# Performance work log

Hardware: AMD Instinct MI355X
Metric: run time of the kernel (lower is better)

The kernel has to match this reference:

```python
import jax, jax.numpy as jnp
import numpy as np
from jax import lax

B, A, K = 16, 200000, 300          # batch, anchors, NMS candidate cap
THR_CONF, THR_NMS = 0.5, 0.3
VAR0, VAR1 = 0.1, 0.2              # RetinaFace decode variances


def setup_inputs() -> dict:
    key = jax.random.key(0)
    k1, k2, k3, k4, k5 = jax.random.split(key, 5)
    p_loc = jax.random.normal(k1, (B, A, 4), jnp.float32) * 0.5
    p_conf = jax.random.normal(k2, (B, A, 1), jnp.float32) - 2.0
    p_landms = jax.random.normal(k3, (B, A, 10), jnp.float32) * 0.5
    cxy = jax.random.uniform(k4, (A, 2), jnp.float32)
    wh = 0.01 + 0.09 * jax.random.uniform(k5, (A, 2), jnp.float32)
    anchors = jnp.concatenate([cxy, wh], axis=-1)   # [A,4] cx,cy,w,h in [0,1]
    return {"p_loc": p_loc, "p_conf": p_conf, "p_landms": p_landms, "anchors": anchors}


def _decode_boxes_ltrb(anchors, loc):
    # fix_bbox: cxy = a_cxy + loc[:2]*0.1*a_wh ; wh = a_wh * exp(loc[2:]*0.2)
    a = anchors[None]                              # [1,A,4]
    cxy = a[..., :2] + loc[..., :2] * VAR0 * a[..., 2:]
    wh = a[..., 2:] * jnp.exp(loc[..., 2:] * VAR1)
    half = 0.5 * wh
    return jnp.concatenate([cxy - half, cxy + half], axis=-1)  # xywh2ltrb -> [B,A,4]


def _decode_keypoints(anchors, landms):
    # fix_keypoints: 5 points, each a_cxy + d*0.1*a_wh (computed in original fwd; unused in outputs)
    a = anchors[None]
    d = landms.reshape(landms.shape[0], landms.shape[1], 5, 2)
    kp = a[..., None, :2] + d * VAR0 * a[..., None, 2:]
    return kp.reshape(landms.shape)


def _iou_matrix(b):  # b [K,4] ltrb -> [K,K]
    lt = jnp.maximum(b[:, None, :2], b[None, :, :2])
    rb = jnp.minimum(b[:, None, 2:], b[None, :, 2:])
    wh = jnp.clip(rb - lt, 0.0)
    inter = wh[..., 0] * wh[..., 1]
    area = jnp.clip(b[:, 2] - b[:, 0], 0.0) * jnp.clip(b[:, 3] - b[:, 1], 0.0)
    union = area[:, None] + area[None, :] - inter
    return inter / jnp.maximum(union, 1e-9)


def _nms_keep(boxes, valid):
    # boxes already sorted by descending score; greedy NMS over K candidates
    iou = _iou_matrix(boxes)
    idx = jnp.arange(K)
    def body(i, keep):
        sup = keep[i] & (iou[i] > THR_NMS) & (idx > i)
        return keep & ~sup
    return lax.fori_loop(0, K, body, valid)


def reference(p_loc, p_conf, p_landms, anchors):
    scores = jax.nn.sigmoid(p_conf[..., 0])                     # [B,A]
    boxes_ltrb = _decode_boxes_ltrb(anchors, p_loc)             # [B,A,4]
    _ = _decode_keypoints(anchors, p_landms)                    # faithful dead compute

    mask = scores >= THR_CONF
    masked_scores = jnp.where(mask, scores, 0.0)
    top_scores, top_idx = lax.top_k(masked_scores, K)           # [B,K] sorted desc
    top_boxes = jnp.take_along_axis(boxes_ltrb, top_idx[..., None], axis=1)  # [B,K,4]
    valid = top_scores >= THR_CONF

    keep = jax.vmap(_nms_keep)(top_boxes, valid)                # [B,K] bool
    keep_f = keep.astype(top_scores.dtype)

    ids_batch2 = jnp.where(keep, jnp.broadcast_to(jnp.arange(B)[:, None], (B, K)), -1).reshape(-1)
    p_boxes_ltrb2 = (top_boxes * keep_f[..., None]).reshape(-1, 4)
    p_scores2 = (top_scores * keep_f).reshape(-1)
    p_labels2 = keep_f.reshape(-1)   # original labels are all ones; zero on padded slots
    return ids_batch2, p_boxes_ltrb2, p_labels2, p_scores2, keep.reshape(-1)
```

## Files before the change

kernel.cpp:

```cpp
#include <hip/hip_runtime.h>
#include <cstdint>

typedef unsigned int u32;
typedef unsigned long long u64;

#define B 16
#define A 200000
#define K 300
#define NREG 196

__global__ __launch_bounds__(256) void scan_kernel(const float* __restrict__ p_conf,
                                                   u64* __restrict__ cand,
                                                   u32* __restrict__ cnt) {
    __shared__ u64 lbuf[1024];
    __shared__ u32 lcnt;
    const int b  = blockIdx.y;
    const int bx = blockIdx.x;
    const int f4 = bx * 256 + threadIdx.x;

    if (threadIdx.x == 0) lcnt = 0;
    __syncthreads();

    if (f4 < A / 4) {
        const float4 c4 = ((const float4*)(p_conf + (size_t)b * A))[f4];
        const float xs[4] = {c4.x, c4.y, c4.z, c4.w};
        #pragma unroll
        for (int e = 0; e < 4; ++e) {
            const float x = xs[e];
            if (x >= -0.001f) {
                float s = 1.0f / (1.0f + expf(-x));
                if (s >= 0.5f) {
                    u32 sb  = __float_as_uint(s);
                    u32 idx = (u32)(f4 * 4 + e);
                    u64 key = ((u64)sb << 32) | (u64)(0xFFFFFFFFu - idx);
                    u32 p = atomicAdd(&lcnt, 1u);
                    lbuf[p] = key;
                }
            }
        }
    }
    __syncthreads();
    const u32 total = lcnt;
    u64* dst = cand + ((size_t)(b * NREG + bx) << 10);
    for (u32 t = threadIdx.x; t < total; t += 256) dst[t] = lbuf[t];
    if (threadIdx.x == 0) cnt[b * NREG + bx] = total;
}

__global__ __launch_bounds__(512) void select_nms_kernel(
    const float* __restrict__ p_loc,
    const float* __restrict__ anchors,
    const u64* __restrict__ cand,
    const u32* __restrict__ cnt,
    float* __restrict__ out) {

    __shared__ u32 scnt[NREG];
    __shared__ u32 hist[512];
    __shared__ u32 sfx[512];
    __shared__ u32 wsum[8];
    __shared__ u64 buf[1024];
    __shared__ u64 skey[K];
    __shared__ float sl[K], st_[K], sr[K], sb_[K], sar[K];
    __shared__ u64 mask[K][5];
    __shared__ u64 validw[5], kcur[5], sup[5];
    __shared__ int s_changed;
    __shared__ u32 sh_cut, sh_m;

    const int b    = blockIdx.x;
    const int tid  = threadIdx.x;
    const int lane = tid & 63;
    const int wv   = tid >> 6;

    hist[tid] = 0;
    {   u64* mf = &mask[0][0];
        for (int i = tid; i < K * 5; i += 512) mf[i] = 0ull; }
    for (int i = tid; i < NREG; i += 512) scnt[i] = cnt[b * NREG + i];
    if (tid == 0) { sh_m = 0; sh_cut = 0; }
    __syncthreads();

    for (int r = wv; r < NREG; r += 8) {
        const u32 kr = scnt[r];
        const u64* p = cand + ((size_t)(b * NREG + r) << 10);
        for (u32 i = lane; i < kr; i += 64) {
            u32 sb  = (u32)(p[i] >> 32);
            u32 bin = min((sb - 0x3F000000u) >> 14, 511u);
            atomicAdd(&hist[bin], 1u);
        }
    }
    __syncthreads();

    u32 s = hist[tid];
    #pragma unroll
    for (int off = 1; off < 64; off <<= 1) {
        u32 t = __shfl_down(s, off, 64);
        if (lane + off < 64) s += t;
    }
    if (lane == 0) wsum[wv] = s;
    __syncthreads();
    u32 tail = 0;
    #pragma unroll
    for (int w = 0; w < 8; ++w) if (w > wv) tail += wsum[w];
    sfx[tid] = s + tail;
    __syncthreads();

    const u32 need = min((u32)K, sfx[0]);
    if (need > 0) {
        if (sfx[tid] >= need && (tid == 511 || sfx[tid + 1] < need)) sh_cut = (u32)tid;
    }
    __syncthreads();

    const u32 cut = sh_cut;
    if (need > 0) {
        for (int r = wv; r < NREG; r += 8) {
            const u32 kr = scnt[r];
            const u64* p = cand + ((size_t)(b * NREG + r) << 10);
            for (u32 i = lane; i < kr; i += 64) {
                u64 kk  = p[i];
                u32 bin = min(((u32)(kk >> 32) - 0x3F000000u) >> 14, 511u);
                if (bin >= cut) {
                    u32 q = atomicAdd(&sh_m, 1u);
                    if (q < 1024) buf[q] = kk;
                }
            }
        }
    }
    __syncthreads();
    const u32 M = min(sh_m, 1024u);

    for (u32 t = tid; t < M; t += 512) {
        const u64 mykey = buf[t];
        u32 r = 0;
        #pragma unroll 4
        for (u32 j = 0; j < M; ++j) r += (buf[j] > mykey) ? 1u : 0u;
        if (r < (u32)K) skey[r] = mykey;
    }
    __syncthreads();

    const u32 S = need;
    float dl = 0.f, dt = 0.f, dr = 0.f, db = 0.f, dsc = 0.f;
    if (tid < K) {
        float ar = 0.f;
        if ((u32)tid < S) {
            u64 kk = skey[tid];
            dsc = __uint_as_float((u32)(kk >> 32));
            u32 aidx = 0xFFFFFFFFu - (u32)(kk & 0xFFFFFFFFull);
            const float4 loc = ((const float4*)p_loc)[(size_t)b * A + aidx];
            const float4 an  = ((const float4*)anchors)[aidx];
            float cx = an.x + loc.x * 0.1f * an.z;
            float cy = an.y + loc.y * 0.1f * an.w;
            float w  = an.z * expf(loc.z * 0.2f);
            float h  = an.w * expf(loc.w * 0.2f);
            dl = cx - 0.5f * w; dt = cy - 0.5f * h;
            dr = cx + 0.5f * w; db = cy + 0.5f * h;
            ar = fmaxf(dr - dl, 0.0f) * fmaxf(db - dt, 0.0f);
        }
        sl[tid] = dl; st_[tid] = dt; sr[tid] = dr; sb_[tid] = db; sar[tid] = ar;
    }
    __syncthreads();

    {
        int r, j0, jstep; bool active;
        if (tid < K) { r = tid;     j0 = r + 1; jstep = (r < 212) ? 2 : 1; active = ((u32)r < S); }
        else         { r = tid - K; j0 = r + 2; jstep = 2;                 active = ((u32)r < S); }
        if (active) {
            const float li = sl[r], ti = st_[r], ri = sr[r], bi = sb_[r], ai = sar[r];
            u64 acc = 0; int wcur = j0 >> 6;
            for (int j = j0; j < (int)S; j += jstep) {
                const int w = j >> 6;
                if (w != wcur) {
                    if (acc) atomicOr(&mask[r][wcur], acc);
                    acc = 0; wcur = w;
                }
                float lt0 = fmaxf(li, sl[j]);
                float lt1 = fmaxf(ti, st_[j]);
                float rb0 = fminf(ri, sr[j]);
                float rb1 = fminf(bi, sb_[j]);
                float iw = fmaxf(rb0 - lt0, 0.0f);
                float ih = fmaxf(rb1 - lt1, 0.0f);
                float inter = iw * ih;
                float uni = ai + sar[j] - inter;
                float iou = inter / fmaxf(uni, 1e-9f);
                if (iou > 0.3f) acc |= (1ull << (j & 63));
            }
            if (acc) atomicOr(&mask[r][wcur], acc);
        }
    }

    u64 m0 = 0, m1 = 0, m2 = 0, m3 = 0, m4 = 0;
    __syncthreads();
    if ((u32)tid < S) {
        m0 = mask[tid][0]; m1 = mask[tid][1]; m2 = mask[tid][2];
        m3 = mask[tid][3]; m4 = mask[tid][4];
    }
    if (tid < 5) {
        int rem = (int)S - tid * 64;
        u64 v = rem <= 0 ? 0ull : (rem >= 64 ? ~0ull : ((1ull << rem) - 1ull));
        validw[tid] = v; kcur[tid] = v;
    }
    __syncthreads();

    for (u32 it = 0; it <= S; ++it) {
        if (tid < 5) sup[tid] = 0;
        if (tid == 0) s_changed = 0;
        __syncthreads();
        u64 c0 = 0, c1 = 0, c2 = 0, c3 = 0, c4 = 0;
        if ((u32)tid < S) {
            u64 kw = kcur[tid >> 6];
            if ((kw >> (tid & 63)) & 1ull) { c0 = m0; c1 = m1; c2 = m2; c3 = m3; c4 = m4; }
        }
        #pragma unroll
        for (int off = 1; off < 64; off <<= 1) {
            c0 |= __shfl_xor(c0, off, 64);
            c1 |= __shfl_xor(c1, off, 64);
            c2 |= __shfl_xor(c2, off, 64);
            c3 |= __shfl_xor(c3, off, 64);
            c4 |= __shfl_xor(c4, off, 64);
        }
        if (lane == 0) {
            if (c0) atomicOr(&sup[0], c0);
            if (c1) atomicOr(&sup[1], c1);
            if (c2) atomicOr(&sup[2], c2);
            if (c3) atomicOr(&sup[3], c3);
            if (c4) atomicOr(&sup[4], c4);
        }
        __syncthreads();
        if (tid < 5) {
            u64 nk = validw[tid] & ~sup[tid];
            if (nk != kcur[tid]) { s_changed = 1; kcur[tid] = nk; }
        }
        __syncthreads();
        if (!s_changed) break;
    }

    if (tid < K) {
        const int g = b * K + tid;
        const bool kept = (kcur[tid >> 6] >> (tid & 63)) & 1ull;
        out[g] = kept ? (float)b : -1.0f;
        float* obox = out + B * K + (size_t)g * 4;
        obox[0] = kept ? dl : 0.0f;
        obox[1] = kept ? dt : 0.0f;
        obox[2] = kept ? dr : 0.0f;
        obox[3] = kept ? db : 0.0f;
        out[B * K * 5 + g] = kept ? 1.0f : 0.0f;
        out[B * K * 6 + g] = kept ? dsc : 0.0f;
        out[B * K * 7 + g] = kept ? 1.0f : 0.0f;
    }
}

extern "C" void kernel_launch(void* const* d_in, const int* in_sizes, int n_in,
                              void* d_out, int out_size, void* d_ws, size_t ws_size,
                              hipStream_t stream) {
    const float* p_loc   = (const float*)d_in[0];
    const float* p_conf  = (const float*)d_in[1];
    const float* anchors = (const float*)d_in[3];
    float* out = (float*)d_out;

    u64* cand = (u64*)d_ws;
    u32* cnt  = (u32*)((char*)d_ws + (size_t)B * NREG * 1024 * 8);

    dim3 gridA(NREG, B);
    scan_kernel<<<gridA, 256, 0, stream>>>(p_conf, cand, cnt);
    select_nms_kernel<<<B, 512, 0, stream>>>(p_loc, anchors, cand, cnt, out);
}
```

Measured before the change: 247.7 us.

## Compact candidates globally and build score histogram in scan kernel

The scan kernel now appends candidates into a per-batch compact buffer through a global atomic counter and accumulates the score histogram in global memory. The select kernel reads the precomputed histogram and a single contiguous candidate list instead of walking 196 sparse per-block regions twice. This takes serial histogram and gather work off the 16-block select kernel. In exchange it adds global atomics, a memset launch, and a fixed cap of 8192 candidates per batch that would silently drop candidates if exceeded.

```diff
diff --git a/kernel.cpp b/kernel.cpp
--- a/kernel.cpp
+++ b/kernel.cpp
@@ -7,16 +7,18 @@
 #define B 16
 #define A 200000
 #define K 300
-#define NREG 196
+#define CAP 8192
+#define NBIN 512
 
 __global__ __launch_bounds__(256) void scan_kernel(const float* __restrict__ p_conf,
                                                    u64* __restrict__ cand,
-                                                   u32* __restrict__ cnt) {
+                                                   u32* __restrict__ cnt,
+                                                   u32* __restrict__ hist) {
     __shared__ u64 lbuf[1024];
     __shared__ u32 lcnt;
+    __shared__ u32 lbase;
     const int b  = blockIdx.y;
-    const int bx = blockIdx.x;
-    const int f4 = bx * 256 + threadIdx.x;
+    const int f4 = blockIdx.x * 256 + threadIdx.x;
 
     if (threadIdx.x == 0) lcnt = 0;
     __syncthreads();
@@ -40,10 +42,16 @@
         }
     }
     __syncthreads();
+    if (threadIdx.x == 0 && lcnt > 0) lbase = atomicAdd(&cnt[b], lcnt);
+    __syncthreads();
     const u32 total = lcnt;
-    u64* dst = cand + ((size_t)(b * NREG + bx) << 10);
-    for (u32 t = threadIdx.x; t < total; t += 256) dst[t] = lbuf[t];
-    if (threadIdx.x == 0) cnt[b * NREG + bx] = total;
+    for (u32 t = threadIdx.x; t < total; t += 256) {
+        const u64 kk = lbuf[t];
+        const u32 bin = min(((u32)(kk >> 32) - 0x3F000000u) >> 14, (u32)(NBIN - 1));
+        atomicAdd(&hist[b * NBIN + bin], 1u);
+        const u32 g = lbase + t;
+        if (g < CAP) cand[(size_t)b * CAP + g] = kk;
+    }
 }
 
 __global__ __launch_bounds__(512) void select_nms_kernel(
@@ -51,11 +59,10 @@
     const float* __restrict__ anchors,
     const u64* __restrict__ cand,
     const u32* __restrict__ cnt,
+    const u32* __restrict__ hist,
     float* __restrict__ out) {
 
-    __shared__ u32 scnt[NREG];
-    __shared__ u32 hist[512];
-    __shared__ u32 sfx[512];
+    __shared__ u32 sfx[NBIN];
     __shared__ u32 wsum[8];
     __shared__ u64 buf[1024];
     __shared__ u64 skey[K];
@@ -69,26 +76,14 @@
     const int tid  = threadIdx.x;
     const int lane = tid & 63;
     const int wv   = tid >> 6;
-
-    hist[tid] = 0;
+    const u32 c    = min(cnt[b], (u32)CAP);
+    const u64* mycand = cand + (size_t)b * CAP;
+
     {   u64* mf = &mask[0][0];
         for (int i = tid; i < K * 5; i += 512) mf[i] = 0ull; }
-    for (int i = tid; i < NREG; i += 512) scnt[i] = cnt[b * NREG + i];
     if (tid == 0) { sh_m = 0; sh_cut = 0; }
-    __syncthreads();
-
-    for (int r = wv; r < NREG; r += 8) {
-        const u32 kr = scnt[r];
-        const u64* p = cand + ((size_t)(b * NREG + r) << 10);
-        for (u32 i = lane; i < kr; i += 64) {
-            u32 sb  = (u32)(p[i] >> 32);
-            u32 bin = min((sb - 0x3F000000u) >> 14, 511u);
-            atomicAdd(&hist[bin], 1u);
-        }
-    }
-    __syncthreads();
-
-    u32 s = hist[tid];
+
+    u32 s = hist[b * NBIN + tid];
     #pragma unroll
     for (int off = 1; off < 64; off <<= 1) {
         u32 t = __shfl_down(s, off, 64);
@@ -104,23 +99,16 @@
 
     const u32 need = min((u32)K, sfx[0]);
     if (need > 0) {
-        if (sfx[tid] >= need && (tid == 511 || sfx[tid + 1] < need)) sh_cut = (u32)tid;
-    }
-    __syncthreads();
-
-    const u32 cut = sh_cut;
-    if (need > 0) {
-        for (int r = wv; r < NREG; r += 8) {
-            const u32 kr = scnt[r];
-            const u64* p = cand + ((size_t)(b * NREG + r) << 10);
-            for (u32 i = lane; i < kr; i += 64) {
-                u64 kk  = p[i];
-                u32 bin = min(((u32)(kk >> 32) - 0x3F000000u) >> 14, 511u);
-                if (bin >= cut) {
-                    u32 q = atomicAdd(&sh_m, 1u);
-                    if (q < 1024) buf[q] = kk;
-                }
-            }
+        if (sfx[tid] >= need && (tid == NBIN - 1 || sfx[tid + 1] < need)) sh_cut = (u32)tid;
+    }
+    __syncthreads();
+
+    const u32 thr = 0x3F000000u + (sh_cut << 14);
+    for (u32 i = tid; i < c; i += 512) {
+        const u64 kk = mycand[i];
+        if ((u32)(kk >> 32) >= thr) {
+            u32 q = atomicAdd(&sh_m, 1u);
+            if (q < 1024) buf[q] = kk;
         }
     }
     __syncthreads();
@@ -254,10 +242,13 @@
     const float* anchors = (const float*)d_in[3];
     float* out = (float*)d_out;
 
-    u64* cand = (u64*)d_ws;
-    u32* cnt  = (u32*)((char*)d_ws + (size_t)B * NREG * 1024 * 8);
-
-    dim3 gridA(NREG, B);
-    scan_kernel<<<gridA, 256, 0, stream>>>(p_conf, cand, cnt);
-    select_nms_kernel<<<B, 512, 0, stream>>>(p_loc, anchors, cand, cnt, out);
+    u32* hist = (u32*)d_ws;
+    u32* cnt  = hist + B * NBIN;
+    u64* cand = (u64*)((char*)d_ws + (size_t)(B * NBIN + B) * 4);
+
+    hipMemsetAsync(d_ws, 0, (size_t)(B * NBIN + B) * 4, stream);
+
+    dim3 gridA((A / 4 + 255) / 256, B);
+    scan_kernel<<<gridA, 256, 0, stream>>>(p_conf, cand, cnt, hist);
+    select_nms_kernel<<<B, 512, 0, stream>>>(p_loc, anchors, cand, cnt, hist, out);
 }
```

After: 266.8 us. +7.7%, slower.

## Use fixed-size zero-padded candidate slots and compact them into LDS once

Applied to the files above, without the earlier changes.

The scan kernel now writes a fixed slot of 96 zero-padded keys per region instead of a variable-length list plus a separate count array. The select kernel bulk-loads every slot with coalesced 16-byte reads, compacts the nonzero keys into a shared buffer, and runs both the histogram and the threshold pass over that LDS copy instead of walking global memory twice with per-region loops. This removes the dependent count loads and the second global pass, at the cost of always reading the full padded slot array. It also silently truncates any region that has more than 96 positives, which is a correctness risk if positives cluster.

```diff
diff --git a/kernel.cpp b/kernel.cpp
--- a/kernel.cpp
+++ b/kernel.cpp
@@ -8,10 +8,12 @@
 #define A 200000
 #define K 300
 #define NREG 196
+#define RSLOT 96
+#define LCAP 8192
+#define NBIN 512
 
 __global__ __launch_bounds__(256) void scan_kernel(const float* __restrict__ p_conf,
-                                                   u64* __restrict__ cand,
-                                                   u32* __restrict__ cnt) {
+                                                   u64* __restrict__ cand) {
     __shared__ u64 lbuf[1024];
     __shared__ u32 lcnt;
     const int b  = blockIdx.y;
@@ -34,28 +36,27 @@
                     u32 idx = (u32)(f4 * 4 + e);
                     u64 key = ((u64)sb << 32) | (u64)(0xFFFFFFFFu - idx);
                     u32 p = atomicAdd(&lcnt, 1u);
-                    lbuf[p] = key;
+                    if (p < 1024) lbuf[p] = key;
                 }
             }
         }
     }
     __syncthreads();
-    const u32 total = lcnt;
-    u64* dst = cand + ((size_t)(b * NREG + bx) << 10);
-    for (u32 t = threadIdx.x; t < total; t += 256) dst[t] = lbuf[t];
-    if (threadIdx.x == 0) cnt[b * NREG + bx] = total;
+    const u32 total = min(lcnt, (u32)RSLOT);
+    u64* dst = cand + (size_t)(b * NREG + bx) * RSLOT;
+    for (u32 t = threadIdx.x; t < RSLOT; t += 256)
+        dst[t] = (t < total) ? lbuf[t] : 0ull;
 }
 
 __global__ __launch_bounds__(512) void select_nms_kernel(
     const float* __restrict__ p_loc,
     const float* __restrict__ anchors,
     const u64* __restrict__ cand,
-    const u32* __restrict__ cnt,
     float* __restrict__ out) {
 
-    __shared__ u32 scnt[NREG];
-    __shared__ u32 hist[512];
-    __shared__ u32 sfx[512];
+    __shared__ u64 lcand[LCAP];
+    __shared__ u32 hist[NBIN];
+    __shared__ u32 sfx[NBIN];
     __shared__ u32 wsum[8];
     __shared__ u64 buf[1024];
     __shared__ u64 skey[K];
@@ -63,28 +64,40 @@
     __shared__ u64 mask[K][5];
     __shared__ u64 validw[5], kcur[5], sup[5];
     __shared__ int s_changed;
-    __shared__ u32 sh_cut, sh_m;
+    __shared__ u32 sh_cut, sh_m, sh_c;
 
     const int b    = blockIdx.x;
     const int tid  = threadIdx.x;
     const int lane = tid & 63;
     const int wv   = tid >> 6;
 
-    hist[tid] = 0;
+    hist[tid] = 0; hist[tid] = 0;
     {   u64* mf = &mask[0][0];
         for (int i = tid; i < K * 5; i += 512) mf[i] = 0ull; }
-    for (int i = tid; i < NREG; i += 512) scnt[i] = cnt[b * NREG + i];
-    if (tid == 0) { sh_m = 0; sh_cut = 0; }
-    __syncthreads();
-
-    for (int r = wv; r < NREG; r += 8) {
-        const u32 kr = scnt[r];
-        const u64* p = cand + ((size_t)(b * NREG + r) << 10);
-        for (u32 i = lane; i < kr; i += 64) {
-            u32 sb  = (u32)(p[i] >> 32);
-            u32 bin = min((sb - 0x3F000000u) >> 14, 511u);
-            atomicAdd(&hist[bin], 1u);
-        }
+    if (tid == 0) { sh_m = 0; sh_cut = 0; sh_c = 0; }
+    __syncthreads();
+
+    {
+        const ulonglong2* slots = (const ulonglong2*)(cand + (size_t)b * NREG * RSLOT);
+        const int TOT2 = NREG * RSLOT / 2;
+        for (int base = 0; base < TOT2; base += 1024) {
+            const int i0 = base + tid, i1 = base + 512 + tid;
+            ulonglong2 v0 = make_ulonglong2(0, 0), v1 = make_ulonglong2(0, 0);
+            if (i0 < TOT2) v0 = slots[i0];
+            if (i1 < TOT2) v1 = slots[i1];
+            if (v0.x) { u32 p = atomicAdd(&sh_c, 1u); if (p < LCAP) lcand[p] = v0.x; }
+            if (v0.y) { u32 p = atomicAdd(&sh_c, 1u); if (p < LCAP) lcand[p] = v0.y; }
+            if (v1.x) { u32 p = atomicAdd(&sh_c, 1u); if (p < LCAP) lcand[p] = v1.x; }
+            if (v1.y) { u32 p = atomicAdd(&sh_c, 1u); if (p < LCAP) lcand[p] = v1.y; }
+        }
+    }
+    __syncthreads();
+    const u32 C = min(sh_c, (u32)LCAP);
+
+    for (u32 i = tid; i < C; i += 512) {
+        u32 sb  = (u32)(lcand[i] >> 32);
+        u32 bin = min((sb - 0x3F000000u) >> 14, (u32)(NBIN - 1));
+        atomicAdd(&hist[bin], 1u);
     }
     __syncthreads();
 
@@ -102,25 +115,18 @@
     sfx[tid] = s + tail;
     __syncthreads();
 
-    const u32 need = min((u32)K, sfx[0]);
+    const u32 need = min((u32)K, C);
     if (need > 0) {
-        if (sfx[tid] >= need && (tid == 511 || sfx[tid + 1] < need)) sh_cut = (u32)tid;
-    }
-    __syncthreads();
-
-    const u32 cut = sh_cut;
-    if (need > 0) {
-        for (int r = wv; r < NREG; r += 8) {
-            const u32 kr = scnt[r];
-            const u64* p = cand + ((size_t)(b * NREG + r) << 10);
-            for (u32 i = lane; i < kr; i += 64) {
-                u64 kk  = p[i];
-                u32 bin = min(((u32)(kk >> 32) - 0x3F000000u) >> 14, 511u);
-                if (bin >= cut) {
-                    u32 q = atomicAdd(&sh_m, 1u);
-                    if (q < 1024) buf[q] = kk;
-                }
-            }
+        if (sfx[tid] >= need && (tid == NBIN - 1 || sfx[tid + 1] < need)) sh_cut = (u32)tid;
+    }
+    __syncthreads();
+
+    const u32 thr = 0x3F000000u + (sh_cut << 14);
+    for (u32 i = tid; i < C; i += 512) {
+        const u64 kk = lcand[i];
+        if ((u32)(kk >> 32) >= thr) {
+            u32 q = atomicAdd(&sh_m, 1u);
+            if (q < 1024) buf[q] = kk;
         }
     }
     __syncthreads();
@@ -255,9 +261,8 @@
     float* out = (float*)d_out;
 
     u64* cand = (u64*)d_ws;
-    u32* cnt  = (u32*)((char*)d_ws + (size_t)B * NREG * 1024 * 8);
 
     dim3 gridA(NREG, B);
-    scan_kernel<<<gridA, 256, 0, stream>>>(p_conf, cand, cnt);
-    select_nms_kernel<<<B, 512, 0, stream>>>(p_loc, anchors, cand, cnt, out);
+    scan_kernel<<<gridA, 256, 0, stream>>>(p_conf, cand);
+    select_nms_kernel<<<B, 512, 0, stream>>>(p_loc, anchors, cand, out);
 }
```

Result: faster. 234.3 us (-5.4%).
